# Kernel tuning notes

Hardware: AMD Instinct MI355X
Metric: run time of the kernel (lower is better)

The kernel has to match this reference:

```python
import jax, jax.numpy as jnp
import numpy as np

TEMPERATURE = 0.5


def setup_inputs() -> dict:
    key = jax.random.key(0)
    k1, k2 = jax.random.split(key)
    N, D = 4096, 512
    emb_i = jax.random.normal(k1, (N, D), dtype=jnp.float32)
    emb_j = jax.random.normal(k2, (N, D), dtype=jnp.float32)
    return {"emb_i": emb_i, "emb_j": emb_j}


def reference(emb_i, emb_j):
    # L2-normalize each embedding row (F.normalize, dim=1)
    z_i = emb_i / jnp.linalg.norm(emb_i, axis=1, keepdims=True)
    z_j = emb_j / jnp.linalg.norm(emb_j, axis=1, keepdims=True)
    reps = jnp.concatenate([z_i, z_j], axis=0)  # [2N, D]
    N = emb_i.shape[0]
    M = 2 * N
    # cosine similarity of normalized vectors == dot product -> [2N, 2N]
    sim = jnp.einsum('id,jd->ij', reps, reps) / TEMPERATURE
    # denominator: sum_k!=i exp(sim[i,k]); original multiplies by one-hot complement
    exp_sim = jnp.exp(sim)
    denom = jnp.sum(exp_sim, axis=1) - jnp.diagonal(exp_sim)  # [2N]
    log_denom = jnp.log(denom)
    # positive pairs: (k, k+N) and (k+N, k)
    idx = jnp.arange(N)
    pos_ij = sim[idx, idx + N]          # sim(k, k+N)/T
    pos_ji = sim[idx + N, idx]          # sim(k+N, k)/T
    loss = jnp.sum(-(pos_ij - log_denom[:N]) - (pos_ji - log_denom[N:]))
    return loss / (2.0 * N)
```

## Files before the change

### kernel.cpp

```cpp
#include <hip/hip_runtime.h>
#include <cstdint>
#include <cstddef>

constexpr int N_ROWS = 4096;
constexpr int D      = 512;
constexpr int M      = 8192;
constexpr int NTILE  = 64;
constexpr int NBLK   = NTILE * (NTILE + 1) / 2;
constexpr int BKB    = 128;
constexpr int LDSB   = 128 * BKB;

using f32x4 = __attribute__((ext_vector_type(4))) float;
using i32x4 = __attribute__((ext_vector_type(4))) int;
using i32x8 = __attribute__((ext_vector_type(8))) int;

#define ASYNC_CP16(gsrc, ldst)                                                      \
    __builtin_amdgcn_global_load_lds(                                               \
        (const __attribute__((address_space(1))) unsigned int*)(gsrc),              \
        (__attribute__((address_space(3))) unsigned int*)(ldst), 16, 0, 0)

#define SS_FP8(pk, accum)                                                           \
    do {                                                                            \
        float f0 = __builtin_amdgcn_cvt_f32_fp8((pk), 0);                           \
        float f1 = __builtin_amdgcn_cvt_f32_fp8((pk), 1);                           \
        float f2 = __builtin_amdgcn_cvt_f32_fp8((pk), 2);                           \
        float f3 = __builtin_amdgcn_cvt_f32_fp8((pk), 3);                           \
        (accum) += f0 * f0 + f1 * f1 + f2 * f2 + f3 * f3;                           \
    } while (0)

__global__ __launch_bounds__(256) void normpos_kernel(
    const float* __restrict__ emb_i, const float* __restrict__ emb_j,
    uint8_t* __restrict__ zb, float* __restrict__ diagss,
    float* __restrict__ pos)
{
    const int wave = threadIdx.x >> 6, lane = threadIdx.x & 63;
    const int k = blockIdx.x * 4 + wave;

    const float4* a = (const float4*)(emb_i + (size_t)k * D);
    const float4* b = (const float4*)(emb_j + (size_t)k * D);
    float4 a0 = a[lane * 2], a1 = a[lane * 2 + 1];
    float4 b0 = b[lane * 2], b1 = b[lane * 2 + 1];

    float ssi = a0.x*a0.x + a0.y*a0.y + a0.z*a0.z + a0.w*a0.w
              + a1.x*a1.x + a1.y*a1.y + a1.z*a1.z + a1.w*a1.w;
    float ssj = b0.x*b0.x + b0.y*b0.y + b0.z*b0.z + b0.w*b0.w
              + b1.x*b1.x + b1.y*b1.y + b1.z*b1.z + b1.w*b1.w;
    float dp  = a0.x*b0.x + a0.y*b0.y + a0.z*b0.z + a0.w*b0.w
              + a1.x*b1.x + a1.y*b1.y + a1.z*b1.z + a1.w*b1.w;
    #pragma unroll
    for (int off = 32; off; off >>= 1) {
        ssi += __shfl_xor(ssi, off, 64);
        ssj += __shfl_xor(ssj, off, 64);
        dp  += __shfl_xor(dp,  off, 64);
    }
    const float invi = rsqrtf(ssi), invj = rsqrtf(ssj);

    const float zi[8] = {a0.x*invi, a0.y*invi, a0.z*invi, a0.w*invi,
                         a1.x*invi, a1.y*invi, a1.z*invi, a1.w*invi};
    const float zj[8] = {b0.x*invj, b0.y*invj, b0.z*invj, b0.w*invj,
                         b1.x*invj, b1.y*invj, b1.z*invj, b1.w*invj};

    int pi0 = __builtin_amdgcn_cvt_pk_fp8_f32(zi[0], zi[1], 0, false);
    pi0     = __builtin_amdgcn_cvt_pk_fp8_f32(zi[2], zi[3], pi0, true);
    int pi1 = __builtin_amdgcn_cvt_pk_fp8_f32(zi[4], zi[5], 0, false);
    pi1     = __builtin_amdgcn_cvt_pk_fp8_f32(zi[6], zi[7], pi1, true);
    int pj0 = __builtin_amdgcn_cvt_pk_fp8_f32(zj[0], zj[1], 0, false);
    pj0     = __builtin_amdgcn_cvt_pk_fp8_f32(zj[2], zj[3], pj0, true);
    int pj1 = __builtin_amdgcn_cvt_pk_fp8_f32(zj[4], zj[5], 0, false);
    pj1     = __builtin_amdgcn_cvt_pk_fp8_f32(zj[6], zj[7], pj1, true);

    float dssi = 0.f, dssj = 0.f;
    SS_FP8(pi0, dssi);
    SS_FP8(pi1, dssi);
    SS_FP8(pj0, dssj);
    SS_FP8(pj1, dssj);

    const unsigned long long vi =
        ((unsigned long long)(unsigned)pi1 << 32) | (unsigned)pi0;
    const unsigned long long vj =
        ((unsigned long long)(unsigned)pj1 << 32) | (unsigned)pj0;
    *(unsigned long long*)(zb + (size_t)k * D + lane * 8)            = vi;
    *(unsigned long long*)(zb + (size_t)(k + N_ROWS) * D + lane * 8) = vj;

    #pragma unroll
    for (int off = 32; off; off >>= 1) {
        dssi += __shfl_xor(dssi, off, 64);
        dssj += __shfl_xor(dssj, off, 64);
    }
    if (lane == 0) {
        diagss[k]          = dssi;
        diagss[k + N_ROWS] = dssj;
        pos[k]             = 2.0f * dp * invi * invj;
    }
}

__global__ __launch_bounds__(512, 4) void simgemm_kernel(
    const uint8_t* __restrict__ zb, float* __restrict__ partials)
{
    __shared__ i32x4 AsV[2 * LDSB / 16];
    __shared__ i32x4 BsV[2 * LDSB / 16];
    __shared__ float rp[8][32];
    __shared__ float cp8[8][64];
    uint8_t* As = (uint8_t*)AsV;
    uint8_t* Bs = (uint8_t*)BsV;

    const int tid  = threadIdx.x;
    const int wave = tid >> 6, lane = tid & 63;
    const int l15  = lane & 15, ks = lane >> 4;

    const int t = blockIdx.x;
    int bi = (int)((129.0f - sqrtf(129.0f * 129.0f - 8.0f * (float)t)) * 0.5f);
    while (bi > 0 && bi * (129 - bi) / 2 > t) --bi;
    while ((bi + 1) * (129 - (bi + 1)) / 2 <= t) ++bi;
    const int bj = bi + (t - bi * (129 - bi) / 2);
    const bool diag = (bi == bj);

    const int wrow = (wave >> 1) * 32;
    const int wcol = (wave & 1) * 64;

    const int scol = ((lane & 7) ^ ((lane >> 3) & 7)) * 16;
    const uint8_t* gA = zb + (size_t)(bi * 128 + wave * 16 + (lane >> 3)) * D + scol;
    const uint8_t* gB = zb + (size_t)(bj * 128 + wave * 16 + (lane >> 3)) * D + scol;
    uint8_t* lA = As + wave * 16 * BKB;
    uint8_t* lB = Bs + wave * 16 * BKB;

    #pragma unroll
    for (int c = 0; c < 2; ++c) {
        ASYNC_CP16(gA + (size_t)c * 8 * D, lA + c * 8 * BKB);
        ASYNC_CP16(gB + (size_t)c * 8 * D, lB + c * 8 * BKB);
    }

    f32x4 acc[2][4] = {};
    const int sw  = l15 & 7;
    const int co0 = ((ks * 2)     ^ sw) * 16;
    const int co1 = ((ks * 2 + 1) ^ sw) * 16;

    for (int it = 0; it < D / BKB; ++it) {
        __syncthreads();

        if (it + 1 < D / BKB) {
            const int kc  = (it + 1) * BKB;
            const int off = ((it + 1) & 1) * LDSB;
            #pragma unroll
            for (int c = 0; c < 2; ++c) {
                ASYNC_CP16(gA + kc + (size_t)c * 8 * D, lA + off + c * 8 * BKB);
                ASYNC_CP16(gB + kc + (size_t)c * 8 * D, lB + off + c * 8 * BKB);
            }
        }

        const int cb = (it & 1) * LDSB;
        i32x8 af[2], bg[4];
        #pragma unroll
        for (int f = 0; f < 2; ++f) {
            const uint8_t* base = As + cb + (wrow + f * 16 + l15) * BKB;
            i32x4 lo = *(const i32x4*)(base + co0);
            i32x4 hi = *(const i32x4*)(base + co1);
            af[f] = __builtin_shufflevector(lo, hi, 0, 1, 2, 3, 4, 5, 6, 7);
        }
        #pragma unroll
        for (int f = 0; f < 4; ++f) {
            const uint8_t* base = Bs + cb + (wcol + f * 16 + l15) * BKB;
            i32x4 lo = *(const i32x4*)(base + co0);
            i32x4 hi = *(const i32x4*)(base + co1);
            bg[f] = __builtin_shufflevector(lo, hi, 0, 1, 2, 3, 4, 5, 6, 7);
        }
        #pragma unroll
        for (int i = 0; i < 2; ++i)
            #pragma unroll
            for (int j = 0; j < 4; ++j)
                acc[i][j] = __builtin_amdgcn_mfma_scale_f32_16x16x128_f8f6f4(
                    af[i], bg[j], acc[i][j], 0, 0, 0, 0x7F, 0, 0x7F);
    }

    float rowp[2][4] = {};
    #pragma unroll
    for (int j = 0; j < 4; ++j) {
        float cpj = 0.f;
        #pragma unroll
        for (int i = 0; i < 2; ++i)
            #pragma unroll
            for (int r = 0; r < 4; ++r) {
                float e = __expf(2.0f * acc[i][j][r]);
                rowp[i][r] += e;
                cpj += e;
            }
        if (!diag) {
            cpj += __shfl_xor(cpj, 16, 64);
            cpj += __shfl_xor(cpj, 32, 64);
            if (ks == 0) cp8[wave][j * 16 + l15] = cpj;
        }
    }
    #pragma unroll
    for (int i = 0; i < 2; ++i)
        #pragma unroll
        for (int r = 0; r < 4; ++r) {
            float e = rowp[i][r];
            e += __shfl_xor(e, 1, 64);
            e += __shfl_xor(e, 2, 64);
            e += __shfl_xor(e, 4, 64);
            e += __shfl_xor(e, 8, 64);
            if (l15 == 0) rp[wave][i * 16 + ks * 4 + r] = e;
        }
    __syncthreads();

    float* pA = partials + (size_t)(bi * NTILE + bj) * 128;
    float* pB = partials + (size_t)(bj * NTILE + bi) * 128;
    if (tid < 128) {
        const int m = tid >> 5, rr = tid & 31;
        pA[tid] = rp[m * 2][rr] + rp[m * 2 + 1][rr];
    } else if (tid < 256 && !diag) {
        const int c = tid - 128, h = c >> 6, cc = c & 63;
        pB[c] = cp8[h][cc] + cp8[h + 2][cc] + cp8[h + 4][cc] + cp8[h + 6][cc];
    }
}

__global__ __launch_bounds__(256) void rowfin_kernel(
    const float* __restrict__ partials, const float* __restrict__ diagss,
    const float* __restrict__ pos, float* __restrict__ lgpart)
{
    const int r  = blockIdx.x;
    const int ri = threadIdx.x & 127;
    const int ch = threadIdx.x >> 7;
    const float* base = partials + (size_t)r * NTILE * 128 + ri;
    float s = 0.f;
    #pragma unroll
    for (int c = 0; c < 32; ++c)
        s += base[(size_t)(ch * 32 + c) * 128];
    __shared__ float half1[128];
    __shared__ float red[4];
    if (ch == 1) half1[ri] = s;
    __syncthreads();
    float lg = 0.f;
    if (ch == 0) {
        float rs = s + half1[ri];
        int row = r * 128 + ri;
        lg = __logf(rs - __expf(2.0f * diagss[row]));
    }
    if (threadIdx.x < 64)
        lg -= 2.0f * pos[r * 64 + threadIdx.x];
    #pragma unroll
    for (int off = 32; off; off >>= 1) lg += __shfl_xor(lg, off, 64);
    const int wave = threadIdx.x >> 6, lane = threadIdx.x & 63;
    if (lane == 0) red[wave] = lg;
    __syncthreads();
    if (threadIdx.x == 0) lgpart[r] = red[0] + red[1] + red[2] + red[3];
}

__global__ __launch_bounds__(64) void loss_kernel(
    const float* __restrict__ lgpart, float* __restrict__ out)
{
    float local = lgpart[threadIdx.x];
    #pragma unroll
    for (int off = 32; off; off >>= 1) local += __shfl_xor(local, off, 64);
    if (threadIdx.x == 0) out[0] = local * (1.0f / 8192.0f);
}

extern "C" void kernel_launch(void* const* d_in, const int* in_sizes, int n_in,
                              void* d_out, int out_size, void* d_ws, size_t ws_size,
                              hipStream_t stream)
{
    const float* emb_i = (const float*)d_in[0];
    const float* emb_j = (const float*)d_in[1];

    uint8_t* zb = (uint8_t*)d_ws;
    float* partials = (float*)((char*)d_ws + (size_t)M * D);
    float* diagss   = partials + (size_t)NTILE * NTILE * 128;
    float* pos      = diagss + M;
    float* lgpart   = pos + N_ROWS;
    float* out      = (float*)d_out;

    normpos_kernel<<<N_ROWS / 4, 256, 0, stream>>>(emb_i, emb_j, zb, diagss, pos);
    simgemm_kernel<<<NBLK, 512, 0, stream>>>(zb, partials);
    rowfin_kernel<<<NTILE, 256, 0, stream>>>(partials, diagss, pos, lgpart);
    loss_kernel<<<1, 64, 0, stream>>>(lgpart, out);
}
```

Baseline: 106.8 us.

## Stage full K tile in LDS at once and fuse final loss via atomics

The similarity GEMM now copies the entire 512-byte K extent of both 128-row tiles into about 131 KB of dynamic LDS in one pass. It then runs the four MFMA k-steps after a single barrier, replacing the double-buffered loop and its per-iteration syncs. The separate loss kernel is removed: the row-finalize kernel atomically adds its scaled partial into the output, which normpos zeroes first. The large LDS footprint limits residency to about one block per CU and gives up overlap of loads with compute. The atomic float sum makes the summation order nondeterministic.

```diff
diff --git a/kernel.cpp b/kernel.cpp
--- a/kernel.cpp
+++ b/kernel.cpp
@@ -7,8 +7,6 @@
 constexpr int M      = 8192;
 constexpr int NTILE  = 64;
 constexpr int NBLK   = NTILE * (NTILE + 1) / 2;
-constexpr int BKB    = 128;
-constexpr int LDSB   = 128 * BKB;
 
 using f32x4 = __attribute__((ext_vector_type(4))) float;
 using i32x4 = __attribute__((ext_vector_type(4))) int;
@@ -31,10 +29,11 @@
 __global__ __launch_bounds__(256) void normpos_kernel(
     const float* __restrict__ emb_i, const float* __restrict__ emb_j,
     uint8_t* __restrict__ zb, float* __restrict__ diagss,
-    float* __restrict__ pos)
+    float* __restrict__ pos, float* __restrict__ out)
 {
     const int wave = threadIdx.x >> 6, lane = threadIdx.x & 63;
     const int k = blockIdx.x * 4 + wave;
+    if (blockIdx.x == 0 && threadIdx.x == 0) out[0] = 0.0f;
 
     const float4* a = (const float4*)(emb_i + (size_t)k * D);
     const float4* b = (const float4*)(emb_j + (size_t)k * D);
@@ -94,15 +93,14 @@
     }
 }
 
-__global__ __launch_bounds__(512, 4) void simgemm_kernel(
+__global__ __launch_bounds__(512, 2) void simgemm_kernel(
     const uint8_t* __restrict__ zb, float* __restrict__ partials)
 {
-    __shared__ i32x4 AsV[2 * LDSB / 16];
-    __shared__ i32x4 BsV[2 * LDSB / 16];
-    __shared__ float rp[8][32];
-    __shared__ float cp8[8][64];
-    uint8_t* As = (uint8_t*)AsV;
-    uint8_t* Bs = (uint8_t*)BsV;
+    extern __shared__ uint8_t lds[];
+    uint8_t* As = lds;
+    uint8_t* Bs = lds + 64 * 1024;
+    float*   rp  = (float*)(lds + 128 * 1024);
+    float*   cp8 = (float*)(lds + 128 * 1024 + 1024);
 
     const int tid  = threadIdx.x;
     const int wave = tid >> 6, lane = tid & 63;
@@ -118,50 +116,40 @@
     const int wrow = (wave >> 1) * 32;
     const int wcol = (wave & 1) * 64;
 
-    const int scol = ((lane & 7) ^ ((lane >> 3) & 7)) * 16;
-    const uint8_t* gA = zb + (size_t)(bi * 128 + wave * 16 + (lane >> 3)) * D + scol;
-    const uint8_t* gB = zb + (size_t)(bj * 128 + wave * 16 + (lane >> 3)) * D + scol;
-    uint8_t* lA = As + wave * 16 * BKB;
-    uint8_t* lB = Bs + wave * 16 * BKB;
-
-    #pragma unroll
-    for (int c = 0; c < 2; ++c) {
-        ASYNC_CP16(gA + (size_t)c * 8 * D, lA + c * 8 * BKB);
-        ASYNC_CP16(gB + (size_t)c * 8 * D, lB + c * 8 * BKB);
-    }
+    const int lrow = lane >> 5;
+    const int lch  = lane & 31;
+    const uint8_t* gA0 = zb + (size_t)(bi * 128 + wave * 16 + lrow) * D;
+    const uint8_t* gB0 = zb + (size_t)(bj * 128 + wave * 16 + lrow) * D;
+    uint8_t* lA = As + wave * 16 * 512;
+    uint8_t* lB = Bs + wave * 16 * 512;
+    #pragma unroll
+    for (int m = 0; m < 8; ++m) {
+        const int swm = (2 * m + lrow) & 7;
+        const size_t so = (size_t)(2 * m) * D + (size_t)((lch ^ swm) * 16);
+        ASYNC_CP16(gA0 + so, lA + 2 * m * 512);
+        ASYNC_CP16(gB0 + so, lB + 2 * m * 512);
+    }
+    __syncthreads();
 
     f32x4 acc[2][4] = {};
-    const int sw  = l15 & 7;
-    const int co0 = ((ks * 2)     ^ sw) * 16;
-    const int co1 = ((ks * 2 + 1) ^ sw) * 16;
-
-    for (int it = 0; it < D / BKB; ++it) {
-        __syncthreads();
-
-        if (it + 1 < D / BKB) {
-            const int kc  = (it + 1) * BKB;
-            const int off = ((it + 1) & 1) * LDSB;
-            #pragma unroll
-            for (int c = 0; c < 2; ++c) {
-                ASYNC_CP16(gA + kc + (size_t)c * 8 * D, lA + off + c * 8 * BKB);
-                ASYNC_CP16(gB + kc + (size_t)c * 8 * D, lB + off + c * 8 * BKB);
-            }
-        }
-
-        const int cb = (it & 1) * LDSB;
+    const int sws = l15 & 7;
+    #pragma unroll
+    for (int kk = 0; kk < 4; ++kk) {
+        const int p0 = (kk * 8 + ((2 * ks)     ^ sws)) * 16;
+        const int p1 = (kk * 8 + ((2 * ks + 1) ^ sws)) * 16;
         i32x8 af[2], bg[4];
         #pragma unroll
         for (int f = 0; f < 2; ++f) {
-            const uint8_t* base = As + cb + (wrow + f * 16 + l15) * BKB;
-            i32x4 lo = *(const i32x4*)(base + co0);
-            i32x4 hi = *(const i32x4*)(base + co1);
+            const uint8_t* base = As + (wrow + f * 16 + l15) * 512;
+            i32x4 lo = *(const i32x4*)(base + p0);
+            i32x4 hi = *(const i32x4*)(base + p1);
             af[f] = __builtin_shufflevector(lo, hi, 0, 1, 2, 3, 4, 5, 6, 7);
         }
         #pragma unroll
         for (int f = 0; f < 4; ++f) {
-            const uint8_t* base = Bs + cb + (wcol + f * 16 + l15) * BKB;
-            i32x4 lo = *(const i32x4*)(base + co0);
-            i32x4 hi = *(const i32x4*)(base + co1);
+            const uint8_t* base = Bs + (wcol + f * 16 + l15) * 512;
+            i32x4 lo = *(const i32x4*)(base + p0);
+            i32x4 hi = *(const i32x4*)(base + p1);
             bg[f] = __builtin_shufflevector(lo, hi, 0, 1, 2, 3, 4, 5, 6, 7);
         }
         #pragma unroll
@@ -187,7 +175,7 @@
         if (!diag) {
             cpj += __shfl_xor(cpj, 16, 64);
             cpj += __shfl_xor(cpj, 32, 64);
-            if (ks == 0) cp8[wave][j * 16 + l15] = cpj;
+            if (ks == 0) cp8[wave * 64 + j * 16 + l15] = cpj;
         }
     }
     #pragma unroll
@@ -199,24 +187,25 @@
             e += __shfl_xor(e, 2, 64);
             e += __shfl_xor(e, 4, 64);
             e += __shfl_xor(e, 8, 64);
-            if (l15 == 0) rp[wave][i * 16 + ks * 4 + r] = e;
+            if (l15 == 0) rp[wave * 32 + i * 16 + ks * 4 + r] = e;
         }
     __syncthreads();
 
     float* pA = partials + (size_t)(bi * NTILE + bj) * 128;
     float* pB = partials + (size_t)(bj * NTILE + bi) * 128;
     if (tid < 128) {
-        const int m = tid >> 5, rr = tid & 31;
-        pA[tid] = rp[m * 2][rr] + rp[m * 2 + 1][rr];
+        const int mm = tid >> 5, rr = tid & 31;
+        pA[tid] = rp[mm * 2 * 32 + rr] + rp[(mm * 2 + 1) * 32 + rr];
     } else if (tid < 256 && !diag) {
         const int c = tid - 128, h = c >> 6, cc = c & 63;
-        pB[c] = cp8[h][cc] + cp8[h + 2][cc] + cp8[h + 4][cc] + cp8[h + 6][cc];
+        pB[c] = cp8[h * 64 + cc] + cp8[(h + 2) * 64 + cc]
+              + cp8[(h + 4) * 64 + cc] + cp8[(h + 6) * 64 + cc];
     }
 }
 
 __global__ __launch_bounds__(256) void rowfin_kernel(
     const float* __restrict__ partials, const float* __restrict__ diagss,
-    const float* __restrict__ pos, float* __restrict__ lgpart)
+    const float* __restrict__ pos, float* __restrict__ out)
 {
     const int r  = blockIdx.x;
     const int ri = threadIdx.x & 127;
@@ -243,16 +232,8 @@
     const int wave = threadIdx.x >> 6, lane = threadIdx.x & 63;
     if (lane == 0) red[wave] = lg;
     __syncthreads();
-    if (threadIdx.x == 0) lgpart[r] = red[0] + red[1] + red[2] + red[3];
-}
-
-__global__ __launch_bounds__(64) void loss_kernel(
-    const float* __restrict__ lgpart, float* __restrict__ out)
-{
-    float local = lgpart[threadIdx.x];
-    #pragma unroll
-    for (int off = 32; off; off >>= 1) local += __shfl_xor(local, off, 64);
-    if (threadIdx.x == 0) out[0] = local * (1.0f / 8192.0f);
+    if (threadIdx.x == 0)
+        atomicAdd(out, (red[0] + red[1] + red[2] + red[3]) * (1.0f / 8192.0f));
 }
 
 extern "C" void kernel_launch(void* const* d_in, const int* in_sizes, int n_in,
@@ -266,11 +247,10 @@
     float* partials = (float*)((char*)d_ws + (size_t)M * D);
     float* diagss   = partials + (size_t)NTILE * NTILE * 128;
     float* pos      = diagss + M;
-    float* lgpart   = pos + N_ROWS;
     float* out      = (float*)d_out;
 
-    normpos_kernel<<<N_ROWS / 4, 256, 0, stream>>>(emb_i, emb_j, zb, diagss, pos);
-    simgemm_kernel<<<NBLK, 512, 0, stream>>>(zb, partials);
-    rowfin_kernel<<<NTILE, 256, 0, stream>>>(partials, diagss, pos, lgpart);
-    loss_kernel<<<1, 64, 0, stream>>>(lgpart, out);
-}
+    normpos_kernel<<<N_ROWS / 4, 256, 0, stream>>>(emb_i, emb_j, zb, diagss,
+                                                   pos, out);
+    simgemm_kernel<<<NBLK, 512, 134144, stream>>>(zb, partials);
+    rowfin_kernel<<<NTILE, 256, 0, stream>>>(partials, diagss, pos, out);
+}
```

Measured after the change: 121.2 us. 13.5% more time.
